# Kernel tuning notes

Measured on AMD Instinct MI355X. Metric: run time of the kernel, lower is better.

## Reference

```python
import jax, jax.numpy as jnp
import numpy as np

BETA, GAMMA, DELTA = 1.0, 1.0, 0.0
MEAN = True

def setup_inputs() -> dict:
    key = jax.random.key(0)
    k1, k2 = jax.random.split(key)
    preds = jax.random.normal(k1, (8, 2048, 3), dtype=jnp.float32)
    gts = jax.random.normal(k2, (8, 8192, 3), dtype=jnp.float32)
    return {"preds": preds, "gts": gts}

def _pairwise_dist(x, y):
    # x: [b, n, d], y: [b, m, d] -> P: [b, n, m] squared euclidean
    xx = jnp.sum(x * x, axis=-1)                      # [b, n]
    yy = jnp.sum(y * y, axis=-1)                      # [b, m]
    zz = jnp.einsum('bnd,bmd->bnm', x, y)             # [b, n, m]
    return xx[:, :, None] + yy[:, None, :] - 2.0 * zz

def reference(preds, gts):
    # P[b, i_gt, j_pred]
    P = _pairwise_dist(gts, preds)
    num_generated = P.shape[2]

    mins_over_gt = jnp.min(P, axis=1)                 # [b, m] nearest-gt dist per pred
    loss_m = jnp.mean(jnp.max(mins_over_gt, axis=1))  # max coverage term
    red = jnp.mean if MEAN else jnp.sum
    loss_1 = jnp.mean(red(mins_over_gt, axis=1))

    mins_over_pred = jnp.min(P, axis=2)               # [b, n] nearest-pred dist per gt
    loss_2 = jnp.mean(red(mins_over_pred, axis=1))

    return loss_1 + (GAMMA + DELTA * num_generated) * loss_2 + BETA * loss_m
```

## Files before the change

kernel.cpp:

```cpp
#include <hip/hip_runtime.h>


#define BB 8
#define MM 2048
#define NN 8192

typedef float v2f __attribute__((ext_vector_type(2)));

__device__ __forceinline__ int pad_idx(int q) { return q + (q >> 3); }

__global__ __launch_bounds__(256, 4) void pair_k(const float* __restrict__ preds,
                                                 const float* __restrict__ gts,
                                                 float* __restrict__ rowpart,
                                                 float* __restrict__ colpart,
                                                 float* __restrict__ acc,
                                                 unsigned* __restrict__ bmax,
                                                 unsigned* __restrict__ cnt) {
    const int blk   = blockIdx.x;
    const int b     = blk >> 7;
    const int gtblk = (blk >> 1) & 63;
    const int ph    = blk & 1;
    const int tid   = threadIdx.x;
    const int tx    = tid >> 4;
    const int ty    = tid & 15;

    if (blk == 0 && tid < 16) {
        if (tid == 0) { acc[0] = 0.0f; cnt[0] = 0u; }
        if (tid < 8) bmax[tid] = 0u;
    }

    __shared__ float4 sp4[1152];

    {
        const float4* pg = (const float4*)(preds + (size_t)(b * MM + ph * 1024) * 3);
        float4 r0 = pg[tid * 3 + 0], r1 = pg[tid * 3 + 1], r2 = pg[tid * 3 + 2];
        float x[4], y[4], z[4];
        x[0] = r0.x; y[0] = r0.y; z[0] = r0.z;
        x[1] = r0.w; y[1] = r1.x; z[1] = r1.y;
        x[2] = r1.z; y[2] = r1.w; z[2] = r2.x;
        x[3] = r2.y; y[3] = r2.z; z[3] = r2.w;
#pragma unroll
        for (int k = 0; k < 4; ++k) {
            const int q = tid * 4 + k;
            sp4[pad_idx(q)] = make_float4(-2.0f * x[k], -2.0f * y[k], -2.0f * z[k],
                                          fmaf(x[k], x[k], fmaf(y[k], y[k], z[k] * z[k])));
        }
    }

    v2f gx2[4], gy2[4], gz2[4], gg2[4], rmin2[4];
    {
        const float4* g4 = (const float4*)(gts + (size_t)(b * NN + gtblk * 128 + ty * 8) * 3);
        float4 a0 = g4[0], a1 = g4[1], a2 = g4[2], a3 = g4[3], a4 = g4[4], a5 = g4[5];
        float gx[8], gy[8], gz[8];
        gx[0] = a0.x; gy[0] = a0.y; gz[0] = a0.z;
        gx[1] = a0.w; gy[1] = a1.x; gz[1] = a1.y;
        gx[2] = a1.z; gy[2] = a1.w; gz[2] = a2.x;
        gx[3] = a2.y; gy[3] = a2.z; gz[3] = a2.w;
        gx[4] = a3.x; gy[4] = a3.y; gz[4] = a3.z;
        gx[5] = a3.w; gy[5] = a4.x; gz[5] = a4.y;
        gx[6] = a4.z; gy[6] = a4.w; gz[6] = a5.x;
        gx[7] = a5.y; gy[7] = a5.z; gz[7] = a5.w;
#pragma unroll
        for (int ip = 0; ip < 4; ++ip) {
            gx2[ip] = (v2f){gx[2 * ip], gx[2 * ip + 1]};
            gy2[ip] = (v2f){gy[2 * ip], gy[2 * ip + 1]};
            gz2[ip] = (v2f){gz[2 * ip], gz[2 * ip + 1]};
            gg2[ip] = __builtin_elementwise_fma(gx2[ip], gx2[ip],
                      __builtin_elementwise_fma(gy2[ip], gy2[ip], gz2[ip] * gz2[ip]));
            rmin2[ip] = (v2f){3.4e38f, 3.4e38f};
        }
    }

    __syncthreads();

    for (int step = 0; step < 8; ++step) {
        v2f cmin2[8];
#pragma unroll
        for (int j = 0; j < 8; ++j) cmin2[j] = (v2f){3.4e38f, 3.4e38f};

#pragma unroll
        for (int j = 0; j < 8; ++j) {
            const float4 p = sp4[pad_idx(step * 128 + tx * 8 + j)];
            const v2f px2 = (v2f){p.x, p.x};
            const v2f py2 = (v2f){p.y, p.y};
            const v2f pz2 = (v2f){p.z, p.z};
            const v2f pp2 = (v2f){p.w, p.w};
#pragma unroll
            for (int ip = 0; ip < 4; ++ip) {
                v2f t = __builtin_elementwise_fma(gx2[ip], px2, pp2);
                t     = __builtin_elementwise_fma(gy2[ip], py2, t);
                t     = __builtin_elementwise_fma(gz2[ip], pz2, t);
                v2f d = gg2[ip] + t;
                rmin2[ip] = __builtin_elementwise_min(rmin2[ip], d);
                cmin2[j]  = __builtin_elementwise_min(cmin2[j], d);
            }
        }

        float cmin[8];
#pragma unroll
        for (int j = 0; j < 8; ++j) cmin[j] = fminf(cmin2[j].x, cmin2[j].y);
#pragma unroll
        for (int m = 1; m < 16; m <<= 1) {
#pragma unroll
            for (int j = 0; j < 8; ++j)
                cmin[j] = fminf(cmin[j], __shfl_xor(cmin[j], m, 64));
        }
        if (ty == 0) {
            float4* dst = (float4*)&colpart[((size_t)b * 64 + gtblk) * MM +
                                            ph * 1024 + step * 128 + tx * 8];
            dst[0] = make_float4(cmin[0], cmin[1], cmin[2], cmin[3]);
            dst[1] = make_float4(cmin[4], cmin[5], cmin[6], cmin[7]);
        }
    }

    float* red = (float*)sp4;
    __syncthreads();
#pragma unroll
    for (int ip = 0; ip < 4; ++ip) {
        red[tx * 128 + ty * 8 + 2 * ip]     = rmin2[ip].x;
        red[tx * 128 + ty * 8 + 2 * ip + 1] = rmin2[ip].y;
    }
    __syncthreads();
    if (tid < 128) {
        float m = red[tid];
#pragma unroll
        for (int k = 1; k < 16; ++k) m = fminf(m, red[k * 128 + tid]);
        rowpart[((size_t)b * 2 + ph) * NN + gtblk * 128 + tid] = m;
    }
}

__global__ __launch_bounds__(256) void red_k(const float* __restrict__ rowpart,
                                             const float* __restrict__ colpart,
                                             float* __restrict__ acc,
                                             unsigned* __restrict__ bmax,
                                             unsigned* __restrict__ cnt,
                                             float* __restrict__ out) {
    const int b = blockIdx.x, y = blockIdx.y, tid = threadIdx.x;
    __shared__ float a1[4], a2[4];

    if (y < 8) {
        const int p = y * 256 + tid;
        const float* cp = colpart + (size_t)b * 64 * MM + p;
        float m = 3.4e38f;
#pragma unroll 8
        for (int g = 0; g < 64; ++g) m = fminf(m, cp[(size_t)g * MM]);
        float s = m, mx = m;
#pragma unroll
        for (int o = 32; o > 0; o >>= 1) {
            s += __shfl_down(s, o, 64);
            mx = fmaxf(mx, __shfl_down(mx, o, 64));
        }
        const int w = tid >> 6, lane = tid & 63;
        if (lane == 0) { a1[w] = s; a2[w] = mx; }
        __syncthreads();
        if (tid == 0) {
            float cs = a1[0] + a1[1] + a1[2] + a1[3];
            float cm = fmaxf(fmaxf(a2[0], a2[1]), fmaxf(a2[2], a2[3]));
            atomicAdd(acc, cs / (float)(BB * MM));
            atomicMax(&bmax[b], __float_as_uint(cm));
        }
    } else {
        const float* r = rowpart + (size_t)b * 2 * NN;
        float s = 0.0f;
        for (int i = tid; i < NN; i += 256) s += fminf(r[i], r[NN + i]);
#pragma unroll
        for (int o = 32; o > 0; o >>= 1) s += __shfl_down(s, o, 64);
        const int w = tid >> 6, lane = tid & 63;
        if (lane == 0) a1[w] = s;
        __syncthreads();
        if (tid == 0)
            atomicAdd(acc, (a1[0] + a1[1] + a1[2] + a1[3]) / (float)(BB * NN));
    }

    if (tid == 0) {
        __threadfence();
        unsigned old = atomicAdd(cnt, 1u);
        if (old == 71u) {
            __threadfence();
            float a = atomicAdd(acc, 0.0f);
            float mm = 0.0f;
#pragma unroll
            for (int bb = 0; bb < 8; ++bb)
                mm += __uint_as_float(atomicMax(&bmax[bb], 0u));
            out[0] = a + mm / (float)BB;
        }
    }
}

extern "C" void kernel_launch(void* const* d_in, const int* in_sizes, int n_in,
                              void* d_out, int out_size, void* d_ws, size_t ws_size,
                              hipStream_t stream) {
    const float* preds = (const float*)d_in[0];
    const float* gts   = (const float*)d_in[1];
    float* out = (float*)d_out;

    float* rowpart = (float*)d_ws;
    float* colpart = rowpart + (size_t)2 * BB * NN;
    float* acc     = colpart + (size_t)BB * 64 * MM;
    unsigned* bmax = (unsigned*)(acc + 1);
    unsigned* cnt  = bmax + 8;

    pair_k<<<1024, 256, 0, stream>>>(preds, gts, rowpart, colpart, acc, bmax, cnt);
    red_k<<<dim3(BB, 9), 256, 0, stream>>>(rowpart, colpart, acc, bmax, cnt, out);
}
```

Baseline: 96.08 us.

## Retile pair kernel to 16 gts x 4 preds per thread and defer pred norm

Each thread now keeps 16 ground-truth points in registers and processes 4 predictions per step, instead of 8 and 8. This shrinks the cross-lane column-min reduction from 4 shuffle stages over 8 values to 3 stages over 4 values. The prediction squared norm is added after the column min rather than per pair, which saves an add on that path. In exchange, register use rises from the larger per-thread gt set and the final row-min reduction reads 32 partial rows instead of 16.

```diff
diff --git a/kernel.cpp b/kernel.cpp
--- a/kernel.cpp
+++ b/kernel.cpp
@@ -4,6 +4,7 @@
 #define BB 8
 #define MM 2048
 #define NN 8192
+#define FINF 3.4e38f
 
 typedef float v2f __attribute__((ext_vector_type(2)));
 
@@ -21,8 +22,8 @@
     const int gtblk = (blk >> 1) & 63;
     const int ph    = blk & 1;
     const int tid   = threadIdx.x;
-    const int tx    = tid >> 4;
-    const int ty    = tid & 15;
+    const int tx    = tid >> 3;
+    const int ty    = tid & 7;
 
     if (blk == 0 && tid < 16) {
         if (tid == 0) { acc[0] = 0.0f; cnt[0] = 0u; }
@@ -47,84 +48,83 @@
         }
     }
 
-    v2f gx2[4], gy2[4], gz2[4], gg2[4], rmin2[4];
+    v2f gx2[8], gy2[8], gz2[8], gg2[8];
+    float rmin[16];
     {
-        const float4* g4 = (const float4*)(gts + (size_t)(b * NN + gtblk * 128 + ty * 8) * 3);
-        float4 a0 = g4[0], a1 = g4[1], a2 = g4[2], a3 = g4[3], a4 = g4[4], a5 = g4[5];
-        float gx[8], gy[8], gz[8];
-        gx[0] = a0.x; gy[0] = a0.y; gz[0] = a0.z;
-        gx[1] = a0.w; gy[1] = a1.x; gz[1] = a1.y;
-        gx[2] = a1.z; gy[2] = a1.w; gz[2] = a2.x;
-        gx[3] = a2.y; gy[3] = a2.z; gz[3] = a2.w;
-        gx[4] = a3.x; gy[4] = a3.y; gz[4] = a3.z;
-        gx[5] = a3.w; gy[5] = a4.x; gz[5] = a4.y;
-        gx[6] = a4.z; gy[6] = a4.w; gz[6] = a5.x;
-        gx[7] = a5.y; gy[7] = a5.z; gz[7] = a5.w;
-#pragma unroll
-        for (int ip = 0; ip < 4; ++ip) {
-            gx2[ip] = (v2f){gx[2 * ip], gx[2 * ip + 1]};
-            gy2[ip] = (v2f){gy[2 * ip], gy[2 * ip + 1]};
-            gz2[ip] = (v2f){gz[2 * ip], gz[2 * ip + 1]};
+        float f[48];
+        const float4* g4 = (const float4*)(gts + (size_t)(b * NN + gtblk * 128 + ty * 16) * 3);
+#pragma unroll
+        for (int k = 0; k < 12; ++k) ((float4*)f)[k] = g4[k];
+#pragma unroll
+        for (int ip = 0; ip < 8; ++ip) {
+            const float x0 = f[6 * ip + 0], y0 = f[6 * ip + 1], z0 = f[6 * ip + 2];
+            const float x1 = f[6 * ip + 3], y1 = f[6 * ip + 4], z1 = f[6 * ip + 5];
+            gx2[ip] = (v2f){x0, x1};
+            gy2[ip] = (v2f){y0, y1};
+            gz2[ip] = (v2f){z0, z1};
             gg2[ip] = __builtin_elementwise_fma(gx2[ip], gx2[ip],
                       __builtin_elementwise_fma(gy2[ip], gy2[ip], gz2[ip] * gz2[ip]));
-            rmin2[ip] = (v2f){3.4e38f, 3.4e38f};
+            rmin[2 * ip]     = FINF;
+            rmin[2 * ip + 1] = FINF;
         }
     }
 
     __syncthreads();
 
     for (int step = 0; step < 8; ++step) {
-        v2f cmin2[8];
-#pragma unroll
-        for (int j = 0; j < 8; ++j) cmin2[j] = (v2f){3.4e38f, 3.4e38f};
-
-#pragma unroll
-        for (int j = 0; j < 8; ++j) {
-            const float4 p = sp4[pad_idx(step * 128 + tx * 8 + j)];
-            const v2f px2 = (v2f){p.x, p.x};
-            const v2f py2 = (v2f){p.y, p.y};
-            const v2f pz2 = (v2f){p.z, p.z};
-            const v2f pp2 = (v2f){p.w, p.w};
-#pragma unroll
-            for (int ip = 0; ip < 4; ++ip) {
-                v2f t = __builtin_elementwise_fma(gx2[ip], px2, pp2);
-                t     = __builtin_elementwise_fma(gy2[ip], py2, t);
-                t     = __builtin_elementwise_fma(gz2[ip], pz2, t);
-                v2f d = gg2[ip] + t;
-                rmin2[ip] = __builtin_elementwise_min(rmin2[ip], d);
-                cmin2[j]  = __builtin_elementwise_min(cmin2[j], d);
+        float cmu[4] = {FINF, FINF, FINF, FINF};
+        float pw[4];
+
+#pragma unroll
+        for (int jp = 0; jp < 2; ++jp) {
+            const int j0 = jp * 2, j1 = jp * 2 + 1;
+            const float4 p0 = sp4[pad_idx(step * 128 + tx * 4 + j0)];
+            const float4 p1 = sp4[pad_idx(step * 128 + tx * 4 + j1)];
+            pw[j0] = p0.w; pw[j1] = p1.w;
+            const v2f p0x = (v2f){p0.x, p0.x}, p0y = (v2f){p0.y, p0.y}, p0z = (v2f){p0.z, p0.z};
+            const v2f p1x = (v2f){p1.x, p1.x}, p1y = (v2f){p1.y, p1.y}, p1z = (v2f){p1.z, p1.z};
+            const v2f pp0 = (v2f){p0.w, p0.w}, pp1 = (v2f){p1.w, p1.w};
+
+#pragma unroll
+            for (int ip = 0; ip < 8; ++ip) {
+                v2f u0 = __builtin_elementwise_fma(gx2[ip], p0x,
+                         __builtin_elementwise_fma(gy2[ip], p0y,
+                         __builtin_elementwise_fma(gz2[ip], p0z, gg2[ip])));
+                v2f u1 = __builtin_elementwise_fma(gx2[ip], p1x,
+                         __builtin_elementwise_fma(gy2[ip], p1y,
+                         __builtin_elementwise_fma(gz2[ip], p1z, gg2[ip])));
+                cmu[j0] = fminf(fminf(cmu[j0], u0.x), u0.y);
+                cmu[j1] = fminf(fminf(cmu[j1], u1.x), u1.y);
+                v2f d0 = u0 + pp0;
+                v2f d1 = u1 + pp1;
+                rmin[2 * ip]     = fminf(fminf(rmin[2 * ip], d0.x), d1.x);
+                rmin[2 * ip + 1] = fminf(fminf(rmin[2 * ip + 1], d0.y), d1.y);
             }
         }
 
-        float cmin[8];
-#pragma unroll
-        for (int j = 0; j < 8; ++j) cmin[j] = fminf(cmin2[j].x, cmin2[j].y);
-#pragma unroll
-        for (int m = 1; m < 16; m <<= 1) {
-#pragma unroll
-            for (int j = 0; j < 8; ++j)
-                cmin[j] = fminf(cmin[j], __shfl_xor(cmin[j], m, 64));
+#pragma unroll
+        for (int m = 1; m < 8; m <<= 1) {
+#pragma unroll
+            for (int j = 0; j < 4; ++j)
+                cmu[j] = fminf(cmu[j], __shfl_xor(cmu[j], m, 64));
         }
         if (ty == 0) {
             float4* dst = (float4*)&colpart[((size_t)b * 64 + gtblk) * MM +
-                                            ph * 1024 + step * 128 + tx * 8];
-            dst[0] = make_float4(cmin[0], cmin[1], cmin[2], cmin[3]);
-            dst[1] = make_float4(cmin[4], cmin[5], cmin[6], cmin[7]);
+                                            ph * 1024 + step * 128 + tx * 4];
+            *dst = make_float4(cmu[0] + pw[0], cmu[1] + pw[1],
+                               cmu[2] + pw[2], cmu[3] + pw[3]);
         }
     }
 
     float* red = (float*)sp4;
     __syncthreads();
 #pragma unroll
-    for (int ip = 0; ip < 4; ++ip) {
-        red[tx * 128 + ty * 8 + 2 * ip]     = rmin2[ip].x;
-        red[tx * 128 + ty * 8 + 2 * ip + 1] = rmin2[ip].y;
-    }
+    for (int i = 0; i < 16; ++i) red[tx * 128 + ty * 16 + i] = rmin[i];
     __syncthreads();
     if (tid < 128) {
         float m = red[tid];
 #pragma unroll
-        for (int k = 1; k < 16; ++k) m = fminf(m, red[k * 128 + tid]);
+        for (int k = 1; k < 32; ++k) m = fminf(m, red[k * 128 + tid]);
         rowpart[((size_t)b * 2 + ph) * NN + gtblk * 128 + tid] = m;
     }
 }
@@ -141,7 +141,7 @@
     if (y < 8) {
         const int p = y * 256 + tid;
         const float* cp = colpart + (size_t)b * 64 * MM + p;
-        float m = 3.4e38f;
+        float m = FINF;
 #pragma unroll 8
         for (int g = 0; g < 64; ++g) m = fminf(m, cp[(size_t)g * MM]);
         float s = m, mx = m;
```

Result: slower. 232.9 us (+142.4%).
